# Performance work log

Hardware: AMD Instinct MI355X
Metric: run time of the kernel (lower is better)

## Reference

```python
import jax, jax.numpy as jnp
import numpy as np

LS = (0, 1, 2)
DIMS = tuple(2 * l + 1 for l in LS)          # (1, 3, 5)
MULS = (128, 64, 32)                          # node irreps multiplicities (= attention*heads)
ATT_MULS = (16, 8, 4)                         # attention_irreps multiplicities per head
N_HEADS = 8
N_IRREPS_ATT = sum(ATT_MULS)                  # 28
ATTN_NORM = 1.0 / np.sqrt(N_IRREPS_ATT)
CG = tuple(1.0 / np.sqrt(d) for d in DIMS)    # l (x) l -> 0e Clebsch-Gordan coefficient
N_NODES = 512
EDGE_ATTR_DIM = 32
NODE_DIM = sum(m * d for m, d in zip(MULS, DIMS))  # 480


def split_irreps(x, muls):
    """Split last axis into per-l blocks [..., mul_l, 2l+1]."""
    out, i = [], 0
    for mul, d in zip(muls, DIMS):
        out.append(x[..., i:i + mul * d].reshape(x.shape[:-1] + (mul, d)))
        i += mul * d
    return out


def merge_irreps(parts):
    return jnp.concatenate([p.reshape(p.shape[:-2] + (-1,)) for p in parts], axis=-1)


def e3_linear(parts, Ws):
    # equivariant linear: mixes multiplicities within each l, 1/sqrt(mul_in) norm
    return [jnp.einsum('nim,io->nom', p, W) / np.sqrt(p.shape[-2])
            for p, W in zip(parts, Ws)]


def setup_inputs() -> dict:
    key = jax.random.key(0)
    ks = jax.random.split(key, 16)
    inp = {
        'node_feat': jax.random.normal(ks[0], (N_NODES, NODE_DIM), jnp.float32),
        'edge_attr': jax.random.normal(ks[1], (N_NODES, N_NODES, EDGE_ATTR_DIM), jnp.float32),
        'edge_sh':   jax.random.normal(ks[2], (N_NODES, N_NODES, sum(DIMS)), jnp.float32),
    }
    i = 3
    for nm in ('Wq', 'Wk', 'Wv'):
        for l, mul in enumerate(MULS):
            inp[f'{nm}{l}'] = jax.random.normal(ks[i], (mul, mul), jnp.float32)
            i += 1
    inp['mW1'] = jax.random.normal(ks[i], (EDGE_ATTR_DIM + 2 * sum(MULS), 64), jnp.float32) * 0.05
    inp['mb1'] = jnp.zeros((64,), jnp.float32)
    inp['mW2'] = jax.random.normal(ks[i + 1], (64, 64), jnp.float32) * 0.1
    inp['mb2'] = jnp.zeros((64,), jnp.float32)
    inp['mW3'] = jax.random.normal(ks[i + 2], (64, N_HEADS), jnp.float32) * 0.1
    inp['mb3'] = jnp.zeros((N_HEADS,), jnp.float32)
    return inp


def reference(node_feat, edge_attr, edge_sh,
              Wq0, Wq1, Wq2, Wk0, Wk1, Wk2, Wv0, Wv1, Wv2,
              mW1, mb1, mW2, mb2, mW3, mb3):
    N = node_feat.shape[0]
    nf = split_irreps(node_feat, MULS)                 # per-l: [N, mul_l, 2l+1]
    sh = split_irreps(edge_sh, (1, 1, 1))              # per-l: [N, N, 1, 2l+1]

    def to_heads(parts):
        return [p.reshape(N, N_HEADS, am, d) for p, am, d in zip(parts, ATT_MULS, DIMS)]

    q = to_heads(e3_linear(nf, (Wq0, Wq1, Wq2)))
    k = to_heads(e3_linear(nf, (Wk0, Wk1, Wk2)))
    v = to_heads(e3_linear(nf, (Wv0, Wv1, Wv2)))

    # node (x) edge_sh -> scalars (0e): same-l inner products, CG = 1/sqrt(2l+1)
    feat_rec = jnp.concatenate(
        [jnp.einsum('rim,rsm->rsi', p, s[..., 0, :]) * c for p, s, c in zip(nf, sh, CG)], axis=-1)
    feat_snd = jnp.concatenate(
        [jnp.einsum('sim,rsm->rsi', p, s[..., 0, :]) * c for p, s, c in zip(nf, sh, CG)], axis=-1)
    edge_feat = jnp.concatenate([edge_attr, feat_rec, feat_snd], axis=-1)  # [N,N,480]

    h = jnp.tanh(edge_feat @ mW1 + mb1)
    h = jnp.tanh(h @ mW2 + mb2)
    edge_weight = h @ mW3 + mb3                        # [N, N, H]

    # elementwise q (x) k -> 0e, summed over irreps (== scaled dot product per head)
    logits = sum(jnp.einsum('rhim,shim->rsh', qp, kp) * c
                 for qp, kp, c in zip(q, k, CG))       # [N, N, H]
    weight = jax.nn.softmax(logits * ATTN_NORM + edge_weight, axis=-2)  # softmax over senders

    # weighted aggregation over senders, per irrep
    upd = [jnp.einsum('rsh,shim->rhim', weight, vp) for vp in v]
    # axis_to_mul: [N, H, mul, d] -> [N, H*mul, d]
    upd = [u.reshape(N, N_HEADS * am, d) for u, am, d in zip(upd, ATT_MULS, DIMS)]

    return node_feat + merge_irreps(upd)               # residual (irreps match)
```

## Files before the change

kernel.cpp:

```cpp
#include <hip/hip_runtime.h>
#include <hip/hip_bf16.h>
#include <stdint.h>


#define NNODES 512
#define NDIM   480

#define QS_OFF    0u
#define KT_OFF    245760u
#define VB_OFF    491520u
#define ARE_OFF   737280u
#define ASN_OFF   884736u
#define WF_OFF    1032192u
#define FLAG_OFF  1040384u
#define L_OFF     1040448u
#define WTQ_OFF   3137600u
#define WTK_OFF   3159104u
#define WTV_OFF   3180608u
#define W1T_OFF   3202112u

typedef float f32x4 __attribute__((ext_vector_type(4)));
typedef short s16x8 __attribute__((ext_vector_type(8)));

__device__ __forceinline__ float bf2f(uint16_t u) {
    return __uint_as_float(((uint32_t)u) << 16);
}
__device__ __forceinline__ uint16_t f2bf(float f) {
    union { __hip_bfloat16 h; uint16_t u; } cv;
    cv.h = __float2bfloat16(f);
    return cv.u;
}
__device__ __forceinline__ uint32_t packbf(float lo, float hi) {
    return ((uint32_t)f2bf(hi) << 16) | (uint32_t)f2bf(lo);
}
__device__ __forceinline__ float ldin(const void* p, size_t i, int f32) {
    return f32 ? ((const float*)p)[i] : bf2f(((const uint16_t*)p)[i]);
}
__device__ __forceinline__ float ftanh(float x) {
    float e = __builtin_amdgcn_exp2f(x * 2.885390081777927f);
    return 1.0f - 2.0f * __builtin_amdgcn_rcpf(e + 1.0f);
}

__global__ __launch_bounds__(64) void kDet(const uint32_t* __restrict__ nf,
                                           int* __restrict__ flag)
{
    int t = threadIdx.x;
    uint32_t x = nf[64 + t];
    int e = (x >> 7) & 0xff;
    int good = (x != 0u) && (e >= 100) && (e <= 140);
    unsigned long long m = __ballot(good);
    if (t == 0) flag[0] = (__popcll(m) < 32) ? 1 : 0;
}

#define NS 16384
__global__ __launch_bounds__(256) void kW(
    const void* __restrict__ mW1, const void* __restrict__ mb1,
    const void* __restrict__ mW2, const void* __restrict__ mb2,
    const void* __restrict__ mW3, const void* __restrict__ mb3,
    const void* __restrict__ Wq0, const void* __restrict__ Wq1, const void* __restrict__ Wq2,
    const void* __restrict__ Wk0, const void* __restrict__ Wk1, const void* __restrict__ Wk2,
    const void* __restrict__ Wv0, const void* __restrict__ Wv1, const void* __restrict__ Wv2,
    float* __restrict__ ws, const int* __restrict__ flagp)
{
    const int f32 = flagp[0];
    const int gt = blockIdx.x * 256 + threadIdx.x;
    float* Wf = ws + WF_OFF;

    for (int i = gt; i < 2048; i += NS) Wf[i] = ldin(mW1, i, f32);
    for (int i = gt; i < 4096; i += NS) {
        int o2 = i >> 6, ii = i & 63;
        Wf[2048 + i] = ldin(mW2, ii * 64 + o2, f32);
    }
    for (int i = gt; i < 512; i += NS) Wf[6144 + i] = ldin(mW3, i, f32);
    for (int i = gt; i < 64; i += NS) Wf[6656 + i] = ldin(mb1, i, f32);
    for (int i = gt; i < 64; i += NS) Wf[6720 + i] = ldin(mb2, i, f32);
    for (int i = gt; i < 8; i += NS)  Wf[6784 + i] = ldin(mb3, i, f32);

    const float e3n0 = 0.08838834764831845f, e3n1 = 0.125f, e3n2 = 0.17677669529663687f;
    const float cg1 = 0.5773502691896258f, cg2 = 0.4472135954999579f;
    const float attn = 0.1889822365046136f;

    const void* Wsrc[9] = {Wq0, Wq1, Wq2, Wk0, Wk1, Wk2, Wv0, Wv1, Wv2};
    float* Wdst[3] = {ws + WTQ_OFF, ws + WTK_OFF, ws + WTV_OFF};
    for (int kind = 0; kind < 3; ++kind) {
        const float f0 = (kind == 0) ? e3n0 * attn : e3n0;
        const float f1 = (kind == 0) ? e3n1 * cg1 * attn : e3n1;
        const float f2 = (kind == 0) ? e3n2 * cg2 * attn : e3n2;
        for (int i = gt; i < 16384; i += NS) {
            int o = i >> 7, ii = i & 127;
            Wdst[kind][i] = ldin(Wsrc[kind * 3], (size_t)ii * 128 + o, f32) * f0;
        }
        for (int i = gt; i < 4096; i += NS) {
            int o = i >> 6, ii = i & 63;
            Wdst[kind][16384 + i] = ldin(Wsrc[kind * 3 + 1], (size_t)ii * 64 + o, f32) * f1;
        }
        for (int i = gt; i < 1024; i += NS) {
            int o = i >> 5, ii = i & 31;
            Wdst[kind][20480 + i] = ldin(Wsrc[kind * 3 + 2], (size_t)ii * 32 + o, f32) * f2;
        }
    }
    float* W1T = ws + W1T_OFF;
    for (int i = gt; i < 30720; i += NS) {
        int o = i / 480, row = i - o * 480;
        float cgv;
        if (row < 160)      cgv = 1.0f;
        else if (row < 224) cgv = cg1;
        else if (row < 256) cgv = cg2;
        else if (row < 384) cgv = 1.0f;
        else if (row < 448) cgv = cg1;
        else                cgv = cg2;
        W1T[i] = ldin(mW1, (size_t)row * 64 + o, f32) * cgv;
    }
}

__global__ __launch_bounds__(256) void kA(
    const void* __restrict__ nfu,
    const float* __restrict__ WtQ, const float* __restrict__ WtK,
    const float* __restrict__ WtV, const float* __restrict__ W1T,
    float* __restrict__ qS, float* __restrict__ kS, float* __restrict__ vB,
    uint32_t* __restrict__ ArecG, uint32_t* __restrict__ AsndG,
    const int* __restrict__ flagp)
{
    const int f32 = flagp[0];
    const int n = blockIdx.x, t = threadIdx.x;
    __shared__ float nfs[480];
    for (int i = t; i < 480; i += 256) nfs[i] = ldin(nfu, (size_t)n * 480 + i, f32);
    __syncthreads();

    for (int idx = t; idx < 1440; idx += 256) {
        int kind = idx / 480, rem = idx - kind * 480;
        int o, m, mul, d, off, am, qoff, sub;
        if (rem < 128)      { o = rem;           m = 0;          mul = 128; d = 1; off = 0;   am = 16; qoff = 0;  sub = 0; }
        else if (rem < 320) { int x = rem - 128; o = x / 3; m = x - o * 3; mul = 64;  d = 3; off = 128; am = 8;  qoff = 16; sub = 16384; }
        else                { int x = rem - 320; o = x / 5; m = x - o * 5; mul = 32;  d = 5; off = 320; am = 4;  qoff = 40; sub = 20480; }
        const float* base = (kind == 0) ? WtQ : (kind == 1) ? WtK : WtV;
        const float4* W4 = reinterpret_cast<const float4*>(base + sub + o * mul);
        const float* nf0 = nfs + off + m;
        float ax = 0.f, ay = 0.f, az = 0.f, aw = 0.f;
        const int n4 = mul >> 2;
        for (int i4 = 0; i4 < n4; ++i4) {
            float4 w = W4[i4];
            int ib = 4 * i4 * d;
            ax += nf0[ib]         * w.x;
            ay += nf0[ib + d]     * w.y;
            az += nf0[ib + 2 * d] * w.z;
            aw += nf0[ib + 3 * d] * w.w;
        }
        float acc = (ax + ay) + (az + aw);
        if (kind == 2) {
            vB[(size_t)n * 480 + rem] = acc;
        } else {
            int hh = o / am, a = o - hh * am;
            int j = qoff + a * d + m;
            if (kind == 0) qS[(size_t)n * 480 + hh * 60 + j] = acc;
            else           kS[(size_t)n * 480 + hh * 60 + j] = acc;
        }
    }

    if (t < 128) {
        const int src = t >> 6, o = t & 63;
        float a[9];
        #pragma unroll
        for (int mi = 0; mi < 9; ++mi) {
            const int l = (mi == 0) ? 0 : (mi < 4 ? 1 : 2);
            const int m = (mi == 0) ? 0 : (mi < 4 ? mi - 1 : mi - 4);
            const int mul = (l == 0 ? 128 : l == 1 ? 64 : 32);
            const int d = 2 * l + 1;
            const int off = (l == 0 ? 0 : l == 1 ? 128 : 320);
            const int base = (src == 0) ? (l == 0 ? 32 : l == 1 ? 160 : 224)
                                        : (l == 0 ? 256 : l == 1 ? 384 : 448);
            const float4* W4 = reinterpret_cast<const float4*>(W1T + o * 480 + base);
            const float* nf0 = nfs + off + m;
            float ax = 0.f, ay = 0.f, az = 0.f, aw = 0.f;
            const int n4 = mul >> 2;
            for (int i4 = 0; i4 < n4; ++i4) {
                float4 w = W4[i4];
                int ib = 4 * i4 * d;
                ax += nf0[ib]         * w.x;
                ay += nf0[ib + d]     * w.y;
                az += nf0[ib + 2 * d] * w.z;
                aw += nf0[ib + 3 * d] * w.w;
            }
            a[mi] = (ax + ay) + (az + aw);
        }
        float b[9];
        #pragma unroll
        for (int mi = 0; mi < 9; ++mi) b[mi] = __shfl_xor(a[mi], 1, 64);
        if ((o & 1) == 0) {
            uint32_t* dst = (src ? AsndG : ArecG) + (size_t)n * 288 + (o >> 1);
            #pragma unroll
            for (int mi = 0; mi < 9; ++mi)
                dst[mi * 32] = ((uint32_t)f2bf(b[mi]) << 16) | (uint32_t)f2bf(a[mi]);
        }
    }
}

__global__ __launch_bounds__(256, 4) void kB(
    const void* __restrict__ eaG, const void* __restrict__ shG,
    const uint32_t* __restrict__ ArecG, const uint32_t* __restrict__ AsndG,
    const float* __restrict__ qS, const float* __restrict__ kS,
    const float* __restrict__ Wf, float* __restrict__ L,
    const int* __restrict__ flagp)
{
    __shared__ __align__(16) uint32_t smem[10240];
    uint32_t* ArecS = smem;
    uint32_t* AsndS = smem + 4672;
    float* ewS = (float*)(smem + 8192);
    const int f32 = flagp[0];
    const int t = threadIdx.x;
    const int s0 = blockIdx.x * 16, r0 = blockIdx.y * 16;
    const int lane = t & 63, wv = t >> 6;
    const int g = lane >> 4, nl = lane & 15;

    const int rl = t >> 4, sl = t & 15;
    const int r = r0 + rl, s = s0 + sl;
    const size_t eidx = (((size_t)r) << 9) + s;

    uint32_t eaR[16];
    if (f32) {
        const float4* ep = reinterpret_cast<const float4*>((const float*)eaG + eidx * 32);
        #pragma unroll
        for (int i = 0; i < 8; ++i) {
            float4 v = ep[i];
            eaR[2 * i]     = ((uint32_t)f2bf(v.y) << 16) | (uint32_t)f2bf(v.x);
            eaR[2 * i + 1] = ((uint32_t)f2bf(v.w) << 16) | (uint32_t)f2bf(v.z);
        }
    } else {
        const uint4* ep = reinterpret_cast<const uint4*>((const uint32_t*)eaG + eidx * 16);
        #pragma unroll
        for (int i = 0; i < 4; ++i) {
            uint4 v = ep[i];
            eaR[4 * i] = v.x; eaR[4 * i + 1] = v.y; eaR[4 * i + 2] = v.z; eaR[4 * i + 3] = v.w;
        }
    }

    float sh0, sh1, sh2, sh3, sh4, sh5, sh6, sh7, sh8;
    {
        const size_t sb = eidx * 9;
        if (f32) {
            const float* shp = (const float*)shG + sb;
            sh0 = shp[0]; sh1 = shp[1]; sh2 = shp[2]; sh3 = shp[3]; sh4 = shp[4];
            sh5 = shp[5]; sh6 = shp[6]; sh7 = shp[7]; sh8 = shp[8];
        } else {
            const uint16_t* shp = (const uint16_t*)shG + sb;
            sh0 = bf2f(shp[0]); sh1 = bf2f(shp[1]); sh2 = bf2f(shp[2]);
            sh3 = bf2f(shp[3]); sh4 = bf2f(shp[4]); sh5 = bf2f(shp[5]);
            sh6 = bf2f(shp[6]); sh7 = bf2f(shp[7]); sh8 = bf2f(shp[8]);
        }
    }

    for (int i = t; i < 16 * 288; i += 256) {
        int row = i / 288, c = i - row * 288;
        ArecS[row * 292 + c] = ArecG[(size_t)(r0 + row) * 288 + c];
        AsndS[row * 292 + c] = AsndG[(size_t)(s0 + row) * 288 + c];
    }

    float h[64];
    #pragma unroll
    for (int o = 0; o < 64; ++o) h[o] = Wf[6656 + o];

    __syncthreads();

    {
        const int rb = rl * 292, sb = sl * 292;
        #pragma unroll 1
        for (int mi = 0; mi < 9; ++mi) {
            float shv = sh0;
            shv = (mi == 1) ? sh1 : shv;  shv = (mi == 2) ? sh2 : shv;
            shv = (mi == 3) ? sh3 : shv;  shv = (mi == 4) ? sh4 : shv;
            shv = (mi == 5) ? sh5 : shv;  shv = (mi == 6) ? sh6 : shv;
            shv = (mi == 7) ? sh7 : shv;  shv = (mi == 8) ? sh8 : shv;
            const int ro = rb + mi * 32, so = sb + mi * 32;
            #pragma unroll
            for (int oc = 0; oc < 32; ++oc) {
                uint32_t pa = ArecS[ro + oc];
                uint32_t pb = AsndS[so + oc];
                float a0 = __uint_as_float(pa << 16);
                float b0 = __uint_as_float(pb << 16);
                float a1 = __uint_as_float(pa & 0xffff0000u);
                float b1 = __uint_as_float(pb & 0xffff0000u);
                h[2 * oc]     += shv * (a0 + b0);
                h[2 * oc + 1] += shv * (a1 + b1);
            }
        }
    }

    {
        #pragma unroll 1
        for (int cd = 0; cd < 16; ++cd) {
            uint32_t p = eaR[cd];
            float e0 = __uint_as_float(p << 16);
            float e1 = __uint_as_float(p & 0xffff0000u);
            const float* w0 = Wf + (2 * cd) * 64;
            #pragma unroll
            for (int o = 0; o < 64; ++o) h[o] += e0 * w0[o];
            #pragma unroll
            for (int o = 0; o < 64; ++o) h[o] += e1 * w0[64 + o];
        }
    }

    #pragma unroll
    for (int o = 0; o < 64; ++o) h[o] = ftanh(h[o]);

    __syncthreads();
    #pragma unroll
    for (int c = 0; c < 8; ++c) {
        const int cc = c ^ (t & 7);
        *(uint4*)&smem[t * 32 + cc * 4] =
            make_uint4(packbf(h[c * 8 + 0], h[c * 8 + 1]),
                       packbf(h[c * 8 + 2], h[c * 8 + 3]),
                       packbf(h[c * 8 + 4], h[c * 8 + 5]),
                       packbf(h[c * 8 + 6], h[c * 8 + 7]));
    }
    __builtin_amdgcn_sched_barrier(0);

    s16x8 w2f[4][2];
    #pragma unroll
    for (int nt = 0; nt < 4; ++nt) {
        #pragma unroll
        for (int ks = 0; ks < 2; ++ks) {
            const float* p = Wf + 2048 + (nt * 16 + nl) * 64 + ks * 32 + g * 8;
            s16x8 b;
            #pragma unroll
            for (int j = 0; j < 8; ++j) b[j] = (short)f2bf(p[j]);
            w2f[nt][ks] = b;
        }
    }
    s16x8 w3f[2];
    #pragma unroll
    for (int ks = 0; ks < 2; ++ks) {
        s16x8 b;
        #pragma unroll
        for (int j = 0; j < 8; ++j)
            b[j] = (short)((nl < 8) ? f2bf(Wf[6144 + (ks * 32 + g * 8 + j) * 8 + nl]) : 0);
        w3f[ks] = b;
    }
    float b2v[4];
    #pragma unroll
    for (int nt = 0; nt < 4; ++nt) b2v[nt] = Wf[6720 + nt * 16 + nl];
    const float b3v = (nl < 8) ? Wf[6784 + nl] : 0.f;


    uint16_t* sm16 = (uint16_t*)smem;
    #pragma unroll 1
    for (int mm = 0; mm < 4; ++mm) {
        const int mt = wv * 4 + mm;
        const int row = mt * 16 + nl;
        const int sw0 = ((g    ) ^ (row & 7)) * 4;
        const int sw1 = ((4 + g) ^ (row & 7)) * 4;
        const s16x8 a0 = *(const s16x8*)&smem[row * 32 + sw0];
        const s16x8 a1 = *(const s16x8*)&smem[row * 32 + sw1];
        f32x4 acc[4];
        #pragma unroll
        for (int nt = 0; nt < 4; ++nt) {
            f32x4 a = {b2v[nt], b2v[nt], b2v[nt], b2v[nt]};
            a = __builtin_amdgcn_mfma_f32_16x16x32_bf16(a0, w2f[nt][0], a, 0, 0, 0);
            a = __builtin_amdgcn_mfma_f32_16x16x32_bf16(a1, w2f[nt][1], a, 0, 0, 0);
            acc[nt] = a;
        }
        const int e2base = mt * 16 + g * 4;
        #pragma unroll
        for (int nt = 0; nt < 4; ++nt) {
            const int n = nt * 16 + nl;
            #pragma unroll
            for (int rg = 0; rg < 4; ++rg) {
                const int e2 = e2base + rg;
                const int cc = (n >> 3) ^ (e2 & 7);
                sm16[e2 * 64 + cc * 8 + (n & 7)] = f2bf(ftanh(acc[nt][rg]));
            }
        }
        const s16x8 c0 = *(const s16x8*)&smem[row * 32 + sw0];
        const s16x8 c1 = *(const s16x8*)&smem[row * 32 + sw1];
        f32x4 a3 = {b3v, b3v, b3v, b3v};
        a3 = __builtin_amdgcn_mfma_f32_16x16x32_bf16(c0, w3f[0], a3, 0, 0, 0);
        a3 = __builtin_amdgcn_mfma_f32_16x16x32_bf16(c1, w3f[1], a3, 0, 0, 0);
        if (nl < 8) {
            #pragma unroll
            for (int rg = 0; rg < 4; ++rg) {
                const int e2 = mt * 16 + g * 4 + rg;
                ewS[nl * 256 + (e2 ^ (nl << 2))] = a3[rg];
            }
        }
    }

    __syncthreads();

    for (int task = t; task < 2048; task += 256) {
        const int c    = task & 7;
        const int row  = (task >> 3) & 15;
        const int hh2  = (task >> 7) & 7;
        const int isk  = task >> 10;
        const float* src = (isk ? kS + (size_t)(s0 + row) * 480
                                : qS + (size_t)(r0 + row) * 480) + hh2 * 60 + c * 8;
        const float4 x = *reinterpret_cast<const float4*>(src);
        float4 y = make_float4(0.f, 0.f, 0.f, 0.f);
        if (c < 7) y = *reinterpret_cast<const float4*>(src + 4);
        uint4 p;
        p.x = packbf(x.x, x.y); p.y = packbf(x.z, x.w);
        p.z = packbf(y.x, y.y); p.w = packbf(y.z, y.w);
        *(uint4*)&smem[isk * 4096 + hh2 * 512 + row * 32 + ((c ^ (row & 7)) << 2)] = p;
    }
    __syncthreads();

    {
        const int sw0 = ((g    ) ^ (nl & 7)) << 2;
        const int sw1 = ((4 + g) ^ (nl & 7)) << 2;
        #pragma unroll
        for (int hh2 = 0; hh2 < 2; ++hh2) {
            const int h = wv * 2 + hh2;
            const uint32_t* qb = smem + h * 512;
            const uint32_t* kb = smem + 4096 + h * 512;
            const s16x8 qa0 = *(const s16x8*)&qb[nl * 32 + sw0];
            const s16x8 qa1 = *(const s16x8*)&qb[nl * 32 + sw1];
            const s16x8 ka0 = *(const s16x8*)&kb[nl * 32 + sw0];
            const s16x8 ka1 = *(const s16x8*)&kb[nl * 32 + sw1];
            f32x4 a = {0.f, 0.f, 0.f, 0.f};
            a = __builtin_amdgcn_mfma_f32_16x16x32_bf16(qa0, ka0, a, 0, 0, 0);
            a = __builtin_amdgcn_mfma_f32_16x16x32_bf16(qa1, ka1, a, 0, 0, 0);
            float* Lp = L + (((size_t)h) << 18) + (((size_t)(r0 + g * 4)) << 9) + s0 + nl;
            #pragma unroll
            for (int rg = 0; rg < 4; ++rg) {
                const int e2 = (g * 4 + rg) * 16 + nl;
                Lp[(size_t)rg << 9] = a[rg] + ewS[h * 256 + (e2 ^ (h << 2))];
            }
        }
    }
}

__global__ __launch_bounds__(512) void kAgg(
    const float* __restrict__ L, const float* __restrict__ vB,
    const void* __restrict__ nfu, void* __restrict__ out,
    const int* __restrict__ flagp)
{
    __shared__ float Ls[8192];
    const int f32 = flagp[0];
    const int t = threadIdx.x;
    const int r0 = blockIdx.x * 2;

    {
        const int grp = t >> 5, l = t & 31;
        const int rr = grp >> 3, hsm = grp & 7;
        const float* Lg = L + (((size_t)hsm) << 18) + (((size_t)(r0 + rr)) << 9);
        float v[16];
        float mx = -3.402823466e38f;
        #pragma unroll
        for (int i = 0; i < 16; ++i) {
            v[i] = Lg[l + 32 * i];
            mx = fmaxf(mx, v[i]);
        }
        #pragma unroll
        for (int off = 16; off >= 1; off >>= 1) mx = fmaxf(mx, __shfl_xor(mx, off, 32));
        const float C = 1.4426950408889634f;
        float sm = 0.f;
        #pragma unroll
        for (int i = 0; i < 16; ++i) {
            v[i] = __builtin_amdgcn_exp2f((v[i] - mx) * C);
            sm += v[i];
        }
        #pragma unroll
        for (int off = 16; off >= 1; off >>= 1) sm += __shfl_xor(sm, off, 32);
        const float inv = __builtin_amdgcn_rcpf(sm);
        #pragma unroll
        for (int i = 0; i < 16; ++i)
            Ls[rr * 4096 + (l + 32 * i) * 8 + hsm] = v[i] * inv;
    }
    __syncthreads();

    if (t >= 480) return;
    const int jp = t >> 1, rr = t & 1;
    const int j0 = 2 * jp;
    int hh;
    if (j0 < 128)      hh = j0 >> 4;
    else if (j0 < 320) hh = (j0 - 128) / 24;
    else               hh = (j0 - 320) / 20;

    const float* Lrow = Ls + rr * 4096 + hh;
    float a0 = 0.f, a1 = 0.f;
    const float2* vp = reinterpret_cast<const float2*>(vB + j0);
    #pragma unroll 8
    for (int s = 0; s < 512; ++s) {
        float2 v = vp[(size_t)s * 240];
        float w = Lrow[s * 8];
        a0 += w * v.x; a1 += w * v.y;
    }

    const size_t o0 = (size_t)(r0 + rr) * 480 + j0;
    float r00 = ldin(nfu, o0, f32) + a0;
    float r01 = ldin(nfu, o0 + 1, f32) + a1;
    if (f32) {
        float* op = (float*)out;
        op[o0] = r00; op[o0 + 1] = r01;
    } else {
        uint16_t* op = (uint16_t*)out;
        op[o0] = f2bf(r00); op[o0 + 1] = f2bf(r01);
    }
}

extern "C" void kernel_launch(void* const* d_in, const int* in_sizes, int n_in,
                              void* d_out, int out_size, void* d_ws, size_t ws_size,
                              hipStream_t stream)
{
    (void)in_sizes; (void)n_in; (void)out_size; (void)ws_size;
    const void* nf  = d_in[0];
    const void* eaG = d_in[1];
    const void* shG = d_in[2];

    float* ws = (float*)d_ws;
    float* qS  = ws + QS_OFF;
    float* kS  = ws + KT_OFF;
    float* vB  = ws + VB_OFF;
    uint32_t* ArecG = (uint32_t*)(ws + ARE_OFF);
    uint32_t* AsndG = (uint32_t*)(ws + ASN_OFF);
    float* Wf  = ws + WF_OFF;
    int* flag  = (int*)(ws + FLAG_OFF);
    float* L   = ws + L_OFF;
    float* WtQ = ws + WTQ_OFF;
    float* WtK = ws + WTK_OFF;
    float* WtV = ws + WTV_OFF;
    float* W1T = ws + W1T_OFF;

    kDet<<<1, 64, 0, stream>>>((const uint32_t*)nf, flag);
    kW<<<64, 256, 0, stream>>>(d_in[12], d_in[13], d_in[14], d_in[15], d_in[16], d_in[17],
                               d_in[3], d_in[4], d_in[5], d_in[6], d_in[7], d_in[8],
                               d_in[9], d_in[10], d_in[11], ws, flag);
    kA<<<512, 256, 0, stream>>>(nf, WtQ, WtK, WtV, W1T, qS, kS, vB, ArecG, AsndG, flag);
    kB<<<dim3(32, 32), 256, 0, stream>>>(eaG, shG, ArecG, AsndG, qS, kS, Wf, L, flag);
    kAgg<<<256, 512, 0, stream>>>(L, vB, nf, d_out, flag);
}
```

Baseline: 230.9 us.

## Pre-swizzle q/k to bf16 tiles, pre-pack MLP weights, fold dtype detect into kW

kA now writes q and k directly as bf16 in the swizzled 16-row tile layout that kB's MFMA loads expect. kB can then copy its tiles straight into shared memory with no per-block conversion. The W2 and W3 MLP weights are packed once into per-lane bf16 fragments in kW instead of being converted in every kB block. The dtype-detect kernel is merged into kW, dropping one launch. In kAgg each thread now computes both rows and loads V once for the two. That halves the active threads but reuses the V loads.

Measured after the change: 222.0 us. 1.04x faster.

```diff
diff --git a/kernel.cpp b/kernel.cpp
--- a/kernel.cpp
+++ b/kernel.cpp
@@ -6,8 +6,10 @@
 #define NNODES 512
 #define NDIM   480
 
-#define QS_OFF    0u
-#define KT_OFF    245760u
+#define QG_OFF    0u
+#define W2B_OFF   131072u
+#define W3B_OFF   133120u
+#define KG_OFF    245760u
 #define VB_OFF    491520u
 #define ARE_OFF   737280u
 #define ASN_OFF   884736u
@@ -41,17 +43,6 @@
     return 1.0f - 2.0f * __builtin_amdgcn_rcpf(e + 1.0f);
 }
 
-__global__ __launch_bounds__(64) void kDet(const uint32_t* __restrict__ nf,
-                                           int* __restrict__ flag)
-{
-    int t = threadIdx.x;
-    uint32_t x = nf[64 + t];
-    int e = (x >> 7) & 0xff;
-    int good = (x != 0u) && (e >= 100) && (e <= 140);
-    unsigned long long m = __ballot(good);
-    if (t == 0) flag[0] = (__popcll(m) < 32) ? 1 : 0;
-}
-
 #define NS 16384
 __global__ __launch_bounds__(256) void kW(
     const void* __restrict__ mW1, const void* __restrict__ mb1,
@@ -60,21 +51,49 @@
     const void* __restrict__ Wq0, const void* __restrict__ Wq1, const void* __restrict__ Wq2,
     const void* __restrict__ Wk0, const void* __restrict__ Wk1, const void* __restrict__ Wk2,
     const void* __restrict__ Wv0, const void* __restrict__ Wv1, const void* __restrict__ Wv2,
-    float* __restrict__ ws, const int* __restrict__ flagp)
+    float* __restrict__ ws, const void* __restrict__ nfu, int* __restrict__ flagp)
 {
-    const int f32 = flagp[0];
-    const int gt = blockIdx.x * 256 + threadIdx.x;
+    __shared__ int sflag;
+    const int t = threadIdx.x;
+    if (t < 64) {
+        uint32_t x = ((const uint32_t*)nfu)[64 + t];
+        int e = (x >> 7) & 0xff;
+        int good = (x != 0u) && (e >= 100) && (e <= 140);
+        unsigned long long m = __ballot(good);
+        if (t == 0) sflag = (__popcll(m) < 32) ? 1 : 0;
+    }
+    __syncthreads();
+    const int f32 = sflag;
+    if (blockIdx.x == 0 && t == 0) flagp[0] = f32;
+
+    const int gt = blockIdx.x * 256 + t;
     float* Wf = ws + WF_OFF;
 
     for (int i = gt; i < 2048; i += NS) Wf[i] = ldin(mW1, i, f32);
-    for (int i = gt; i < 4096; i += NS) {
-        int o2 = i >> 6, ii = i & 63;
-        Wf[2048 + i] = ldin(mW2, ii * 64 + o2, f32);
-    }
-    for (int i = gt; i < 512; i += NS) Wf[6144 + i] = ldin(mW3, i, f32);
     for (int i = gt; i < 64; i += NS) Wf[6656 + i] = ldin(mb1, i, f32);
     for (int i = gt; i < 64; i += NS) Wf[6720 + i] = ldin(mb2, i, f32);
     for (int i = gt; i < 8; i += NS)  Wf[6784 + i] = ldin(mb3, i, f32);
+
+    {
+        uint32_t* W2B = (uint32_t*)(ws + W2B_OFF);
+        for (int i = gt; i < 2048; i += NS) {
+            int f = i >> 8, lane = (i >> 2) & 63, w = i & 3;
+            int nt = f >> 1, ks = f & 1, nl2 = lane & 15, gg = lane >> 4;
+            int n = nt * 16 + nl2, kb = ks * 32 + gg * 8 + 2 * w;
+            float lo = ldin(mW2, (size_t)kb * 64 + n, f32);
+            float hi = ldin(mW2, (size_t)(kb + 1) * 64 + n, f32);
+            W2B[i] = packbf(lo, hi);
+        }
+        uint32_t* W3B = (uint32_t*)(ws + W3B_OFF);
+        for (int i = gt; i < 512; i += NS) {
+            int ks = i >> 8, lane = (i >> 2) & 63, w = i & 3;
+            int nl2 = lane & 15, gg = lane >> 4;
+            int kb = ks * 32 + gg * 8 + 2 * w;
+            float lo = (nl2 < 8) ? ldin(mW3, (size_t)kb * 8 + nl2, f32) : 0.f;
+            float hi = (nl2 < 8) ? ldin(mW3, (size_t)(kb + 1) * 8 + nl2, f32) : 0.f;
+            W3B[i] = packbf(lo, hi);
+        }
+    }
 
     const float e3n0 = 0.08838834764831845f, e3n1 = 0.125f, e3n2 = 0.17677669529663687f;
     const float cg1 = 0.5773502691896258f, cg2 = 0.4472135954999579f;
@@ -117,7 +136,7 @@
     const void* __restrict__ nfu,
     const float* __restrict__ WtQ, const float* __restrict__ WtK,
     const float* __restrict__ WtV, const float* __restrict__ W1T,
-    float* __restrict__ qS, float* __restrict__ kS, float* __restrict__ vB,
+    uint32_t* __restrict__ qG, uint32_t* __restrict__ kG, float* __restrict__ vB,
     uint32_t* __restrict__ ArecG, uint32_t* __restrict__ AsndG,
     const int* __restrict__ flagp)
 {
@@ -125,6 +144,14 @@
     const int n = blockIdx.x, t = threadIdx.x;
     __shared__ float nfs[480];
     for (int i = t; i < 480; i += 256) nfs[i] = ldin(nfu, (size_t)n * 480 + i, f32);
+
+    if (t < 64) {
+        const int kind2 = t >> 5, hh = (t >> 2) & 7, j = 60 + (t & 3);
+        const int row = n & 15, rt = n >> 4;
+        const int cc = (j >> 3) ^ (n & 7);
+        uint16_t* dst = (uint16_t*)(kind2 == 0 ? qG : kG);
+        dst[((((size_t)rt * 8 + hh) * 16 + row) * 8 + cc) * 8 + (j & 7)] = 0;
+    }
     __syncthreads();
 
     for (int idx = t; idx < 1440; idx += 256) {
@@ -152,8 +179,10 @@
         } else {
             int hh = o / am, a = o - hh * am;
             int j = qoff + a * d + m;
-            if (kind == 0) qS[(size_t)n * 480 + hh * 60 + j] = acc;
-            else           kS[(size_t)n * 480 + hh * 60 + j] = acc;
+            const int row = n & 15, rt = n >> 4;
+            const int cc = (j >> 3) ^ (n & 7);
+            uint16_t* dst = (uint16_t*)(kind == 0 ? qG : kG);
+            dst[((((size_t)rt * 8 + hh) * 16 + row) * 8 + cc) * 8 + (j & 7)] = f2bf(acc);
         }
     }
 
@@ -198,7 +227,8 @@
 __global__ __launch_bounds__(256, 4) void kB(
     const void* __restrict__ eaG, const void* __restrict__ shG,
     const uint32_t* __restrict__ ArecG, const uint32_t* __restrict__ AsndG,
-    const float* __restrict__ qS, const float* __restrict__ kS,
+    const uint32_t* __restrict__ qG, const uint32_t* __restrict__ kG,
+    const uint32_t* __restrict__ W2B, const uint32_t* __restrict__ W3B,
     const float* __restrict__ Wf, float* __restrict__ L,
     const int* __restrict__ flagp)
 {
@@ -318,23 +348,12 @@
     #pragma unroll
     for (int nt = 0; nt < 4; ++nt) {
         #pragma unroll
-        for (int ks = 0; ks < 2; ++ks) {
-            const float* p = Wf + 2048 + (nt * 16 + nl) * 64 + ks * 32 + g * 8;
-            s16x8 b;
-            #pragma unroll
-            for (int j = 0; j < 8; ++j) b[j] = (short)f2bf(p[j]);
-            w2f[nt][ks] = b;
-        }
+        for (int ks = 0; ks < 2; ++ks)
+            w2f[nt][ks] = ((const s16x8*)W2B)[(nt * 2 + ks) * 64 + lane];
     }
     s16x8 w3f[2];
-    #pragma unroll
-    for (int ks = 0; ks < 2; ++ks) {
-        s16x8 b;
-        #pragma unroll
-        for (int j = 0; j < 8; ++j)
-            b[j] = (short)((nl < 8) ? f2bf(Wf[6144 + (ks * 32 + g * 8 + j) * 8 + nl]) : 0);
-        w3f[ks] = b;
-    }
+    w3f[0] = ((const s16x8*)W3B)[lane];
+    w3f[1] = ((const s16x8*)W3B)[64 + lane];
     float b2v[4];
     #pragma unroll
     for (int nt = 0; nt < 4; ++nt) b2v[nt] = Wf[6720 + nt * 16 + nl];
@@ -385,20 +404,12 @@
 
     __syncthreads();
 
-    for (int task = t; task < 2048; task += 256) {
-        const int c    = task & 7;
-        const int row  = (task >> 3) & 15;
-        const int hh2  = (task >> 7) & 7;
-        const int isk  = task >> 10;
-        const float* src = (isk ? kS + (size_t)(s0 + row) * 480
-                                : qS + (size_t)(r0 + row) * 480) + hh2 * 60 + c * 8;
-        const float4 x = *reinterpret_cast<const float4*>(src);
-        float4 y = make_float4(0.f, 0.f, 0.f, 0.f);
-        if (c < 7) y = *reinterpret_cast<const float4*>(src + 4);
-        uint4 p;
-        p.x = packbf(x.x, x.y); p.y = packbf(x.z, x.w);
-        p.z = packbf(y.x, y.y); p.w = packbf(y.z, y.w);
-        *(uint4*)&smem[isk * 4096 + hh2 * 512 + row * 32 + ((c ^ (row & 7)) << 2)] = p;
+    {
+        const uint4* qg4 = (const uint4*)qG + (size_t)blockIdx.y * 1024;
+        const uint4* kg4 = (const uint4*)kG + (size_t)blockIdx.x * 1024;
+        uint4* sm4 = (uint4*)smem;
+        for (int i = t; i < 2048; i += 256)
+            sm4[i] = (i < 1024) ? qg4[i] : kg4[i - 1024];
     }
     __syncthreads();
 
@@ -466,33 +477,39 @@
     }
     __syncthreads();
 
-    if (t >= 480) return;
-    const int jp = t >> 1, rr = t & 1;
-    const int j0 = 2 * jp;
+    if (t >= 240) return;
+    const int j0 = 2 * t;
     int hh;
     if (j0 < 128)      hh = j0 >> 4;
     else if (j0 < 320) hh = (j0 - 128) / 24;
     else               hh = (j0 - 320) / 20;
 
-    const float* Lrow = Ls + rr * 4096 + hh;
-    float a0 = 0.f, a1 = 0.f;
+    const float* L0 = Ls + hh;
+    const float* L1 = Ls + 4096 + hh;
+    float a0 = 0.f, a1 = 0.f, b0 = 0.f, b1 = 0.f;
     const float2* vp = reinterpret_cast<const float2*>(vB + j0);
     #pragma unroll 8
     for (int s = 0; s < 512; ++s) {
         float2 v = vp[(size_t)s * 240];
-        float w = Lrow[s * 8];
-        a0 += w * v.x; a1 += w * v.y;
-    }
-
-    const size_t o0 = (size_t)(r0 + rr) * 480 + j0;
+        float w0 = L0[s * 8], w1 = L1[s * 8];
+        a0 += w0 * v.x; a1 += w0 * v.y;
+        b0 += w1 * v.x; b1 += w1 * v.y;
+    }
+
+    const size_t o0 = (size_t)r0 * 480 + j0;
+    const size_t o1 = o0 + 480;
     float r00 = ldin(nfu, o0, f32) + a0;
     float r01 = ldin(nfu, o0 + 1, f32) + a1;
+    float r10 = ldin(nfu, o1, f32) + b0;
+    float r11 = ldin(nfu, o1 + 1, f32) + b1;
     if (f32) {
         float* op = (float*)out;
         op[o0] = r00; op[o0 + 1] = r01;
+        op[o1] = r10; op[o1 + 1] = r11;
     } else {
         uint16_t* op = (uint16_t*)out;
         op[o0] = f2bf(r00); op[o0 + 1] = f2bf(r01);
+        op[o1] = f2bf(r10); op[o1 + 1] = f2bf(r11);
     }
 }
 
@@ -506,8 +523,10 @@
     const void* shG = d_in[2];
 
     float* ws = (float*)d_ws;
-    float* qS  = ws + QS_OFF;
-    float* kS  = ws + KT_OFF;
+    uint32_t* qG = (uint32_t*)(ws + QG_OFF);
+    uint32_t* kG = (uint32_t*)(ws + KG_OFF);
+    uint32_t* W2B = (uint32_t*)(ws + W2B_OFF);
+    uint32_t* W3B = (uint32_t*)(ws + W3B_OFF);
     float* vB  = ws + VB_OFF;
     uint32_t* ArecG = (uint32_t*)(ws + ARE_OFF);
     uint32_t* AsndG = (uint32_t*)(ws + ASN_OFF);
@@ -519,11 +538,10 @@
     float* WtV = ws + WTV_OFF;
     float* W1T = ws + W1T_OFF;
 
-    kDet<<<1, 64, 0, stream>>>((const uint32_t*)nf, flag);
     kW<<<64, 256, 0, stream>>>(d_in[12], d_in[13], d_in[14], d_in[15], d_in[16], d_in[17],
                                d_in[3], d_in[4], d_in[5], d_in[6], d_in[7], d_in[8],
-                               d_in[9], d_in[10], d_in[11], ws, flag);
-    kA<<<512, 256, 0, stream>>>(nf, WtQ, WtK, WtV, W1T, qS, kS, vB, ArecG, AsndG, flag);
-    kB<<<dim3(32, 32), 256, 0, stream>>>(eaG, shG, ArecG, AsndG, qS, kS, Wf, L, flag);
+                               d_in[9], d_in[10], d_in[11], ws, nf, flag);
+    kA<<<512, 256, 0, stream>>>(nf, WtQ, WtK, WtV, W1T, qG, kG, vB, ArecG, AsndG, flag);
+    kB<<<dim3(32, 32), 256, 0, stream>>>(eaG, shG, ArecG, AsndG, qG, kG, W2B, W3B, Wf, L, flag);
     kAgg<<<256, 512, 0, stream>>>(L, vB, nf, d_out, flag);
 }
```
